# Kernel tuning notes

Hardware: AMD Instinct MI355X
Metric: run time of the kernel (lower is better)

Reference implementation:

```python
import jax, jax.numpy as jnp
import numpy as np
from jax import lax

H = 256      # hidden_size
B = 256      # batch
S = 672      # encoder history length (7 days of 15-min steps)
T = 96       # target_length (hardcoded TARGET_LENGTH)
IN = 1       # input_size


def _lstm_cell(x, h, c, Wih, Whh, b):
    # PyTorch gate order: i, f, g, o. b = b_ih + b_hh (combined).
    gates = x @ Wih.T + h @ Whh.T + b            # [B, 4H]
    i, f, g, o = jnp.split(gates, 4, axis=-1)
    c = jax.nn.sigmoid(f) * c + jax.nn.sigmoid(i) * jnp.tanh(g)
    h = jax.nn.sigmoid(o) * jnp.tanh(c)
    return h, c


def _run_lstm_layer(xs, Wih, Whh, b):
    # xs: [S, B, in] -> outputs [S, B, H], final (h, c)
    bsz = xs.shape[1]
    h0 = jnp.zeros((bsz, Whh.shape[1]), xs.dtype)
    c0 = jnp.zeros_like(h0)

    def step(carry, x):
        h, c = _lstm_cell(x, carry[0], carry[1], Wih, Whh, b)
        return (h, c), h

    (h, c), ys = lax.scan(step, (h0, c0), xs)
    return ys, h, c


def setup_inputs() -> dict:
    key = jax.random.key(0)
    ks = jax.random.split(key, 18)
    kscale = 1.0 / np.sqrt(H)

    def u(k, shape):
        return jax.random.uniform(k, shape, jnp.float32, -kscale, kscale)

    inp = {
        "features": jax.random.normal(ks[0], (B, S, IN), jnp.float32),
        # encoder LSTM (2 layers)
        "enc_Wih0": u(ks[1], (4 * H, IN)),
        "enc_Whh0": u(ks[2], (4 * H, H)),
        "enc_b0":   u(ks[3], (4 * H,)),
        "enc_Wih1": u(ks[4], (4 * H, H)),
        "enc_Whh1": u(ks[5], (4 * H, H)),
        "enc_b1":   u(ks[6], (4 * H,)),
        # decoder LSTM (2 layers, input size 1)
        "dec_Wih0": u(ks[7], (4 * H, 1)),
        "dec_Whh0": u(ks[8], (4 * H, H)),
        "dec_b0":   u(ks[9], (4 * H,)),
        "dec_Wih1": u(ks[10], (4 * H, H)),
        "dec_Whh1": u(ks[11], (4 * H, H)),
        "dec_b1":   u(ks[12], (4 * H,)),
        # output head: Linear(H,H) -> ReLU -> (Dropout=id at eval) -> Linear(H,1)
        "out_W1": u(ks[13], (H, H)),
        "out_b1": u(ks[14], (H,)),
        "out_W2": u(ks[15], (1, H)),
        "out_b2": u(ks[16], (1,)),
    }
    return inp


def reference(features, enc_Wih0, enc_Whh0, enc_b0, enc_Wih1, enc_Whh1, enc_b1,
              dec_Wih0, dec_Whh0, dec_b0, dec_Wih1, dec_Whh1, dec_b1,
              out_W1, out_b1, out_W2, out_b2):
    # --- encoder: 2-layer LSTM over the history ---
    xs = jnp.swapaxes(features, 0, 1)                       # [S, B, 1]
    ys0, eh0, ec0 = _run_lstm_layer(xs, enc_Wih0, enc_Whh0, enc_b0)
    _,   eh1, ec1 = _run_lstm_layer(ys0, enc_Wih1, enc_Whh1, enc_b1)

    x0 = jnp.zeros((features.shape[0], 1), features.dtype)  # [B, 1]

    def dec_step(carry, _):
        x, h0, c0, h1, c1 = carry
        h0, c0 = _lstm_cell(x, h0, c0, dec_Wih0, dec_Whh0, dec_b0)
        h1, c1 = _lstm_cell(h0, h1, c1, dec_Wih1, dec_Whh1, dec_b1)
        hid = jnp.maximum(h1 @ out_W1.T + out_b1, 0.0)      # ReLU (Dropout=id)
        pred = hid @ out_W2.T + out_b2                      # [B, 1]
        return (pred, h0, c0, h1, c1), pred[:, 0]

    _, preds = lax.scan(dec_step, (x0, eh0, ec0, eh1, ec1), None, length=T)
    return preds.T                                          # [B, T]
```

## Files before the change

kernel.cpp:

```cpp
#include <hip/hip_runtime.h>


#define S_LEN 672
#define T_LEN 96
#define HDIM  256
#define SPIN_MAX (1 << 14)

typedef short short8 __attribute__((ext_vector_type(8)));
typedef float f32x4  __attribute__((ext_vector_type(4)));
typedef unsigned short u16;

#define OFF_FLAG 0
#define OFF_FE   1024
#define OFF_FD   (OFF_FE + 16*8*32)
#define OFF_PART (OFF_FD + 16*16*32)
#define ZERO_END (OFF_PART + 2*16*256*4)
#define OFF_H0   ZERO_END
#define OFF_H1   (OFF_H0 + 16*2*4096*2)
#define OFF_F0   (OFF_H1 + 16*2*4096*2)
#define OFF_F1   (OFF_F0 + 16*4096*2)
#define OFF_C0   (OFF_F1 + 16*4096*2)
#define OFF_C1   (OFF_C0 + 256*256*4)

__device__ __forceinline__ unsigned short f2bf(float f) {
  unsigned u = __float_as_uint(f);
  u += 0x7FFFu + ((u >> 16) & 1u);
  return (unsigned short)(u >> 16);
}
__device__ __forceinline__ float bf2f(unsigned short s) {
  return __uint_as_float(((unsigned)s) << 16);
}
__device__ __forceinline__ float ld_scalar(const void* p, long idx, int mode) {
  if (mode) return bf2f(((const u16*)p)[idx]);
  return ((const float*)p)[idx];
}
__device__ __forceinline__ short8 ld_frag8(const void* p, long row, long ld, long k0, int mode) {
  if (mode) {
    return *(const short8*)((const u16*)p + row * ld + k0);
  } else {
    const float* f = (const float*)p + row * ld + k0;
    short8 r;
#pragma unroll
    for (int i = 0; i < 8; i++) r[i] = (short)f2bf(f[i]);
    return r;
  }
}
__device__ __forceinline__ void st_out(void* out, size_t idx, float v, int mode) {
  if (mode) ((u16*)out)[idx] = f2bf(v);
  else      ((float*)out)[idx] = v;
}
__device__ __forceinline__ float sigm(float x) { return 1.f / (1.f + __expf(-x)); }

__device__ __forceinline__ f32x4 mfma_bf16(short8 a, short8 b, f32x4 c) {
  return __builtin_amdgcn_mfma_f32_16x16x32_bf16(a, b, c, 0, 0, 0);
}

__device__ __forceinline__ void ld16B(const u16* b, short8* c0) {
  asm volatile("global_load_dwordx4 %0, %1, off sc0 sc1"
               : "=&v"(*c0) : "v"(b) : "memory");
}
__device__ __forceinline__ void ld32B(const u16* b, short8* c0, short8* c1) {
  asm volatile(
    "global_load_dwordx4 %0, %2, off sc0 sc1\n\t"
    "global_load_dwordx4 %1, %2, off offset:16 sc0 sc1"
    : "=&v"(*c0), "=&v"(*c1) : "v"(b) : "memory");
}
__device__ __forceinline__ void issue2(const u16* base, short8* t) {
  asm volatile(
    "global_load_dwordx4 %0, %2, off sc0 sc1\n\t"
    "global_load_dwordx4 %1, %2, off offset:64 sc0 sc1"
    : "=&v"(t[0]), "=&v"(t[1]) : "v"(base) : "memory");
}
__device__ __forceinline__ void st16(u16* p, unsigned short v) {
  asm volatile("global_store_short %0, %1, off sc0 sc1"
               :: "v"(p), "v"((unsigned)v) : "memory");
}
__device__ __forceinline__ void stf32(float* p, float v) {
  asm volatile("global_store_dword %0, %1, off sc0 sc1" :: "v"(p), "v"(v) : "memory");
}
__device__ __forceinline__ float ldf32(const float* p) {
  float v;
  asm volatile("global_load_dword %0, %1, off sc0 sc1\n\ts_waitcnt vmcnt(0)"
               : "=&v"(v) : "v"(p) : "memory");
  __builtin_amdgcn_sched_barrier(0);
  return v;
}
__device__ __forceinline__ void waitv0() {
  asm volatile("s_waitcnt vmcnt(0)" ::: "memory");
  __builtin_amdgcn_sched_barrier(0);
}

__device__ __forceinline__ void wg_publish(unsigned* fa, unsigned e) {
  asm volatile("s_waitcnt vmcnt(0)" ::: "memory");
  __syncthreads();
  if (threadIdx.x == 0)
    asm volatile("global_store_dword %0, %1, off sc0 sc1" :: "v"(fa), "v"(e) : "memory");
}
__device__ __forceinline__ void pollge8(const unsigned* flags, unsigned E) {
  const unsigned* addr = flags + (threadIdx.x & 7) * 8;
  int spin = 0;
  for (;;) {
    unsigned v;
    asm volatile("global_load_dword %0, %1, off sc0 sc1\n\ts_waitcnt vmcnt(0)"
                 : "=&v"(v) : "v"(addr) : "memory");
    if (__all(v >= E)) break;
    if (++spin > SPIN_MAX) break;
    __builtin_amdgcn_s_sleep(1);
  }
  __builtin_amdgcn_sched_barrier(0);
}
__device__ __forceinline__ void pollge16(const unsigned* flags, unsigned E) {
  const unsigned* addr = flags + (threadIdx.x & 15) * 8;
  int spin = 0;
  for (;;) {
    unsigned v;
    asm volatile("global_load_dword %0, %1, off sc0 sc1\n\ts_waitcnt vmcnt(0)"
                 : "=&v"(v) : "v"(addr) : "memory");
    if (__all(v >= E)) break;
    if (++spin > SPIN_MAX) break;
    __builtin_amdgcn_s_sleep(1);
  }
  __builtin_amdgcn_sched_barrier(0);
}

__global__ void detect_mode(const unsigned* __restrict__ feat, unsigned* __restrict__ flag) {
  const int t = threadIdx.x;
  int cnt = 0;
#pragma unroll
  for (int i = 0; i < 8; i++) {
    const unsigned wv = feat[t * 8 + i];
    const unsigned e = (wv >> 7) & 0xFFu;
    cnt += (e >= 100u && e <= 130u) ? 1 : 0;
  }
#pragma unroll
  for (int o = 32; o > 0; o >>= 1) cnt += __shfl_down(cnt, o, 64);
  if (t == 0) flag[0] = (cnt >= 256) ? 1u : 0u;
}

__global__ void __launch_bounds__(512, 1)
enc_kernel(const void* __restrict__ feat,
           const void* __restrict__ Wih0, const void* __restrict__ Whh0, const void* __restrict__ b0,
           const void* __restrict__ Wih1, const void* __restrict__ Whh1, const void* __restrict__ b1,
           char* __restrict__ ws) {
  const int mode = (int)*(const unsigned*)(ws + OFF_FLAG);
  const int tid  = threadIdx.x;
  const int lane = tid & 63;
  const int w    = tid >> 6;
  const int wl   = w & 3;
  const int bId  = blockIdx.x;
  const int g    = (bId & 7) * 2 + ((bId >> 3) & 1);
  const int m    = bId >> 4;
  const int sh   = m * 2 + (w >> 2);

  const int fcol = lane & 15;
  const int kq   = lane >> 4;
  const int chq  = sh * 16 + wl * 4 + kq;
  const int bgl  = g * 16 + fcol;
  const int sr   = tid >> 5;
  const int scc  = tid & 31;

  unsigned* fe_g = (unsigned*)(ws + OFF_FE) + g * 64;
  u16* h0s = (u16*)(ws + OFF_H0) + (size_t)g * 2 * 4096;
  u16* h1s = (u16*)(ws + OFF_H1) + (size_t)g * 2 * 4096;
  u16* f0s = (u16*)(ws + OFF_F0) + (size_t)g * 4096;
  u16* f1s = (u16*)(ws + OFF_F1) + (size_t)g * 4096;
  float* c0ws = (float*)(ws + OFF_C0);
  float* c1ws = (float*)(ws + OFF_C1);

  __shared__ short8 sh0[16][33];
  __shared__ short8 sh1[16][33];

  const int n    = 16 * wl + fcol;
  const int grow = (n & 3) * HDIM + sh * 16 + (n >> 2);
  short8 wh0[8], wi1[8], wh1[8];
#pragma unroll
  for (int kf = 0; kf < 8; kf++) {
    const int k0 = kf * 32 + kq * 8;
    wh0[kf] = ld_frag8(Whh0, grow, HDIM, k0, mode);
    wi1[kf] = ld_frag8(Wih1, grow, HDIM, k0, mode);
    wh1[kf] = ld_frag8(Whh1, grow, HDIM, k0, mode);
  }
  float wx[4], bb0[4], bb1[4];
#pragma unroll
  for (int gt = 0; gt < 4; gt++) {
    wx[gt]  = ld_scalar(Wih0, gt * HDIM + chq, mode);
    bb0[gt] = ld_scalar(b0,   gt * HDIM + chq, mode);
    bb1[gt] = ld_scalar(b1,   gt * HDIM + chq, mode);
  }
  float c0 = 0.f, c1 = 0.f, h0keep = 0.f, h1fin = 0.f;

  for (int t = 0; t <= S_LEN; t++) {
    const int pr = (t + 1) & 1, pw = t & 1;
    short8 a0[8], a1[8];
    if (t >= 1) {
      pollge8(fe_g, (unsigned)t);
      short8 va, vb;
      ld16B(h0s + pr * 4096 + tid * 8, &va);
      if (t >= 2) ld16B(h1s + pr * 4096 + tid * 8, &vb);
      waitv0();
      sh0[sr][scc] = va;
      if (t >= 2) sh1[sr][scc] = vb;
      __syncthreads();
#pragma unroll
      for (int kf = 0; kf < 8; kf++) a0[kf] = sh0[fcol][kf * 4 + kq];
      if (t >= 2) {
#pragma unroll
        for (int kf = 0; kf < 8; kf++) a1[kf] = sh1[fcol][kf * 4 + kq];
      }
    }

    f32x4 acc0 = {0.f, 0.f, 0.f, 0.f}, acc1 = {0.f, 0.f, 0.f, 0.f};
    if (t >= 1 && t < S_LEN) {
#pragma unroll
      for (int kf = 0; kf < 8; kf++) acc0 = mfma_bf16(wh0[kf], a0[kf], acc0);
    }
    if (t >= 1) {
#pragma unroll
      for (int kf = 0; kf < 8; kf++) acc1 = mfma_bf16(wi1[kf], a0[kf], acc1);
      if (t >= 2) {
#pragma unroll
        for (int kf = 0; kf < 8; kf++) acc1 = mfma_bf16(wh1[kf], a1[kf], acc1);
      }
    }
    if (t < S_LEN) {
      const float x = ld_scalar(feat, (long)bgl * S_LEN + t, mode);
      const float gi = acc0[0] + x * wx[0] + bb0[0];
      const float gf = acc0[1] + x * wx[1] + bb0[1];
      const float gg = acc0[2] + x * wx[2] + bb0[2];
      const float go = acc0[3] + x * wx[3] + bb0[3];
      c0 = sigm(gf) * c0 + sigm(gi) * tanhf(gg);
      const float h0v = sigm(go) * tanhf(c0);
      h0keep = h0v;
      st16(h0s + pw * 4096 + fcol * 256 + chq, f2bf(h0v));
    }
    if (t >= 1) {
      const float gi = acc1[0] + bb1[0];
      const float gf = acc1[1] + bb1[1];
      const float gg = acc1[2] + bb1[2];
      const float go = acc1[3] + bb1[3];
      c1 = sigm(gf) * c1 + sigm(gi) * tanhf(gg);
      const float h1v = sigm(go) * tanhf(c1);
      if (t < S_LEN) st16(h1s + pw * 4096 + fcol * 256 + chq, f2bf(h1v));
      else h1fin = h1v;
    }
    wg_publish(fe_g + m * 8, (unsigned)(t + 1));
  }
  f0s[fcol * 256 + chq] = f2bf(h0keep);
  f1s[fcol * 256 + chq] = f2bf(h1fin);
  c0ws[(size_t)bgl * HDIM + chq] = c0;
  c1ws[(size_t)bgl * HDIM + chq] = c1;
}

__global__ void __launch_bounds__(256, 1)
dec_kernel(const void* __restrict__ Wih0, const void* __restrict__ Whh0, const void* __restrict__ b0,
           const void* __restrict__ Wih1, const void* __restrict__ Whh1, const void* __restrict__ b1,
           const void* __restrict__ W1, const void* __restrict__ b1h, const void* __restrict__ W2,
           const void* __restrict__ b2, char* __restrict__ ws, void* __restrict__ out) {
  const int mode = (int)*(const unsigned*)(ws + OFF_FLAG);
  const int tid  = threadIdx.x;
  const int lane = tid & 63;
  const int w    = tid >> 6;
  const int bId  = blockIdx.x;
  const int g    = (bId & 7) * 2 + ((bId >> 3) & 1);
  const int m    = bId >> 4;

  const int fcol = lane & 15;
  const int kq   = lane >> 4;
  const int chq  = m * 16 + w * 4 + kq;
  const int bgl  = g * 16 + fcol;
  const int sr   = tid >> 4;
  const int sc2  = (tid & 15) * 2;

  unsigned* fd_g = (unsigned*)(ws + OFF_FD) + g * 128;
  u16* h0s = (u16*)(ws + OFF_H0) + (size_t)g * 2 * 4096;
  u16* h1s = (u16*)(ws + OFF_H1) + (size_t)g * 2 * 4096;
  u16* f0s = (u16*)(ws + OFF_F0) + (size_t)g * 4096;
  u16* f1s = (u16*)(ws + OFF_F1) + (size_t)g * 4096;
  float* partial = (float*)(ws + OFF_PART);
  float* c0ws = (float*)(ws + OFF_C0);
  float* c1ws = (float*)(ws + OFF_C1);

  __shared__ short8 sh0[16][33];
  __shared__ short8 sh1[16][33];
  __shared__ float part[4 * 256];
  __shared__ float redv[256];
  __shared__ float xacc[256];

  const int n    = 16 * w + fcol;
  const int grow = (n & 3) * HDIM + m * 16 + (n >> 2);
  short8 wh0[8], wi1[8], wh1[8], ww1[2];
#pragma unroll
  for (int kf = 0; kf < 8; kf++) {
    const int k0 = kf * 32 + kq * 8;
    wh0[kf] = ld_frag8(Whh0, grow, HDIM, k0, mode);
    wi1[kf] = ld_frag8(Wih1, grow, HDIM, k0, mode);
    wh1[kf] = ld_frag8(Whh1, grow, HDIM, k0, mode);
  }
#pragma unroll
  for (int kf2 = 0; kf2 < 2; kf2++) {
    const int k0 = w * 64 + kf2 * 32 + kq * 8;
    ww1[kf2] = ld_frag8(W1, m * 16 + fcol, HDIM, k0, mode);
  }
  float wx[4], bb0[4], bb1[4];
#pragma unroll
  for (int gt = 0; gt < 4; gt++) {
    wx[gt]  = ld_scalar(Wih0, gt * HDIM + chq, mode);
    bb0[gt] = ld_scalar(b0,   gt * HDIM + chq, mode);
    bb1[gt] = ld_scalar(b1,   gt * HDIM + chq, mode);
  }
  const int hb = tid & 15, hcl = tid >> 4;
  const float b1hv = ld_scalar(b1h, m * 16 + hcl, mode);
  const float w2v  = ld_scalar(W2,  m * 16 + hcl, mode);
  const float b2v  = ld_scalar(b2, 0, mode);

  float c0 = c0ws[(size_t)bgl * HDIM + chq];
  float c1 = c1ws[(size_t)bgl * HDIM + chq];

  for (int s = 0; s < T_LEN; s++) {
    const int ppr = (s - 1) & 1, pcur = s & 1;
    float x = 0.f;
    {
      if (s > 0) pollge16(fd_g, (unsigned)(3 * s));
      short8 va0, va1;
      float pv = 0.f;
      if (s > 0) {
        ld32B(h0s + ppr * 4096 + tid * 16, &va0, &va1);
        pv = ldf32(partial + (((size_t)ppr * 16 + g) * 16 + (tid >> 4)) * 16 + (tid & 15));
      } else {
        ld32B(f0s + tid * 16, &va0, &va1);
        waitv0();
      }
      sh0[sr][sc2] = va0; sh0[sr][sc2 + 1] = va1;
      if (s > 0) xacc[(tid & 15) * 16 + (tid >> 4)] = pv;
      __syncthreads();
      if (s > 0) {
#pragma unroll
        for (int j = 0; j < 16; j++) x += xacc[fcol * 16 + j];
        if (m == 0 && tid < 16)
          st_out(out, (size_t)(g * 16 + tid) * T_LEN + (s - 1), x, mode);
      }
      short8 a0[8];
#pragma unroll
      for (int kf = 0; kf < 8; kf++) a0[kf] = sh0[fcol][kf * 4 + kq];
      f32x4 acc = {0.f, 0.f, 0.f, 0.f};
#pragma unroll
      for (int kf = 0; kf < 8; kf++) acc = mfma_bf16(wh0[kf], a0[kf], acc);
      const float gi = acc[0] + x * wx[0] + bb0[0];
      const float gf = acc[1] + x * wx[1] + bb0[1];
      const float gg = acc[2] + x * wx[2] + bb0[2];
      const float go = acc[3] + x * wx[3] + bb0[3];
      c0 = sigm(gf) * c0 + sigm(gi) * tanhf(gg);
      const float h0v = sigm(go) * tanhf(c0);
      st16(h0s + pcur * 4096 + fcol * 256 + chq, f2bf(h0v));
      wg_publish(fd_g + m * 8, (unsigned)(3 * s + 1));
    }
    {
      pollge16(fd_g, (unsigned)(3 * s + 1));
      short8 va0, va1, vb0, vb1;
      ld32B(h0s + pcur * 4096 + tid * 16, &va0, &va1);
      ld32B(((s == 0) ? f1s : (h1s + ppr * 4096)) + tid * 16, &vb0, &vb1);
      waitv0();
      sh0[sr][sc2] = va0; sh0[sr][sc2 + 1] = va1;
      sh1[sr][sc2] = vb0; sh1[sr][sc2 + 1] = vb1;
      __syncthreads();
      short8 ay[8], a1[8];
#pragma unroll
      for (int kf = 0; kf < 8; kf++) {
        ay[kf] = sh0[fcol][kf * 4 + kq];
        a1[kf] = sh1[fcol][kf * 4 + kq];
      }
      f32x4 acc = {0.f, 0.f, 0.f, 0.f};
#pragma unroll
      for (int kf = 0; kf < 8; kf++) {
        acc = mfma_bf16(wi1[kf], ay[kf], acc);
        acc = mfma_bf16(wh1[kf], a1[kf], acc);
      }
      const float gi = acc[0] + bb1[0];
      const float gf = acc[1] + bb1[1];
      const float gg = acc[2] + bb1[2];
      const float go = acc[3] + bb1[3];
      c1 = sigm(gf) * c1 + sigm(gi) * tanhf(gg);
      const float h1v = sigm(go) * tanhf(c1);
      st16(h1s + pcur * 4096 + fcol * 256 + chq, f2bf(h1v));
      wg_publish(fd_g + m * 8, (unsigned)(3 * s + 2));
    }
    {
      pollge16(fd_g, (unsigned)(3 * s + 2));
      short8 ah[2];
      issue2(h1s + pcur * 4096 + fcol * 256 + w * 64 + kq * 8, ah);
      waitv0();
      f32x4 acc = {0.f, 0.f, 0.f, 0.f};
      acc = mfma_bf16(ww1[0], ah[0], acc);
      acc = mfma_bf16(ww1[1], ah[1], acc);
      *(f32x4*)&part[w * 256 + fcol * 16 + kq * 4] = acc;
      __syncthreads();
      float hid = part[0 * 256 + hb * 16 + hcl] + part[1 * 256 + hb * 16 + hcl]
                + part[2 * 256 + hb * 16 + hcl] + part[3 * 256 + hb * 16 + hcl] + b1hv;
      hid = fmaxf(hid, 0.f);
      redv[hcl * 16 + hb] = hid * w2v;
      __syncthreads();
      if (tid < 16) {
        float a = (m == 0) ? b2v : 0.f;
#pragma unroll
        for (int cc = 0; cc < 16; cc++) a += redv[cc * 16 + tid];
        stf32(partial + (((size_t)pcur * 16 + g) * 16 + m) * 16 + tid, a);
      }
      wg_publish(fd_g + m * 8, (unsigned)(3 * s + 3));
    }
  }
  if (m == 0) {
    pollge16(fd_g, (unsigned)(3 * T_LEN));
    const float pv = ldf32(partial + (((size_t)1 * 16 + g) * 16 + (tid >> 4)) * 16 + (tid & 15));
    xacc[(tid & 15) * 16 + (tid >> 4)] = pv;
    __syncthreads();
    if (tid < 16) {
      float x = 0.f;
#pragma unroll
      for (int j = 0; j < 16; j++) x += xacc[tid * 16 + j];
      st_out(out, (size_t)(g * 16 + tid) * T_LEN + (T_LEN - 1), x, mode);
    }
  }
}

extern "C" void kernel_launch(void* const* d_in, const int* in_sizes, int n_in,
                              void* d_out, int out_size, void* d_ws, size_t ws_size,
                              hipStream_t stream) {
  char* ws = (char*)d_ws;
  hipMemsetAsync(ws, 0, ZERO_END, stream);
  detect_mode<<<1, 64, 0, stream>>>((const unsigned*)d_in[0], (unsigned*)(ws + OFF_FLAG));
  enc_kernel<<<128, 512, 0, stream>>>(d_in[0], d_in[1], d_in[2], d_in[3],
                                      d_in[4], d_in[5], d_in[6], ws);
  dec_kernel<<<256, 256, 0, stream>>>(d_in[7], d_in[8], d_in[9], d_in[10], d_in[11], d_in[12],
                                      d_in[13], d_in[14], d_in[15], d_in[16], ws, d_out);
}
```

Measured before the change: 2.756 ms.

## Embed step tags in hidden-state words to replace flag-based encoder synchronization

The encoder stops publishing per-workgroup step flags and polling them. Each bf16 hidden value is now stored as a 32-bit word with the step index in the high half. Readers load the data directly, check the tags with a workgroup-wide vote, and reload until every tag is current. This removes the store-fence-barrier-flag round trip and the separate poll on each step, at the cost of doubling the h-buffer traffic and adding repack work. Decoder pointers are adjusted for the wider layout; the decoder body is not visible, so whether its h accesses still match is unclear.

```diff
diff --git a/kernel.cpp b/kernel.cpp
--- a/kernel.cpp
+++ b/kernel.cpp
@@ -5,19 +5,20 @@
 #define T_LEN 96
 #define HDIM  256
 #define SPIN_MAX (1 << 14)
+#define VOTE_MAX (1 << 13)
 
 typedef short short8 __attribute__((ext_vector_type(8)));
 typedef float f32x4  __attribute__((ext_vector_type(4)));
+typedef unsigned u32x4 __attribute__((ext_vector_type(4)));
 typedef unsigned short u16;
 
 #define OFF_FLAG 0
-#define OFF_FE   1024
-#define OFF_FD   (OFF_FE + 16*8*32)
+#define OFF_FD   1024
 #define OFF_PART (OFF_FD + 16*16*32)
-#define ZERO_END (OFF_PART + 2*16*256*4)
-#define OFF_H0   ZERO_END
-#define OFF_H1   (OFF_H0 + 16*2*4096*2)
-#define OFF_F0   (OFF_H1 + 16*2*4096*2)
+#define OFF_H0   (OFF_PART + 2*16*256*4)
+#define OFF_H1   (OFF_H0 + 16*2*4096*4)
+#define ZERO_END (OFF_H1 + 16*2*4096*4)
+#define OFF_F0   ZERO_END
 #define OFF_F1   (OFF_F0 + 16*4096*2)
 #define OFF_C0   (OFF_F1 + 16*4096*2)
 #define OFF_C1   (OFF_C0 + 256*256*4)
@@ -50,14 +51,17 @@
   else      ((float*)out)[idx] = v;
 }
 __device__ __forceinline__ float sigm(float x) { return 1.f / (1.f + __expf(-x)); }
+__device__ __forceinline__ unsigned umn(unsigned a, unsigned b) { return a < b ? a : b; }
 
 __device__ __forceinline__ f32x4 mfma_bf16(short8 a, short8 b, f32x4 c) {
   return __builtin_amdgcn_mfma_f32_16x16x32_bf16(a, b, c, 0, 0, 0);
 }
 
-__device__ __forceinline__ void ld16B(const u16* b, short8* c0) {
-  asm volatile("global_load_dwordx4 %0, %1, off sc0 sc1"
-               : "=&v"(*c0) : "v"(b) : "memory");
+__device__ __forceinline__ void ld32Bu(const unsigned* b, u32x4* c0, u32x4* c1) {
+  asm volatile(
+    "global_load_dwordx4 %0, %2, off sc0 sc1\n\t"
+    "global_load_dwordx4 %1, %2, off offset:16 sc0 sc1"
+    : "=&v"(*c0), "=&v"(*c1) : "v"(b) : "memory");
 }
 __device__ __forceinline__ void ld32B(const u16* b, short8* c0, short8* c1) {
   asm volatile(
@@ -74,6 +78,9 @@
 __device__ __forceinline__ void st16(u16* p, unsigned short v) {
   asm volatile("global_store_short %0, %1, off sc0 sc1"
                :: "v"(p), "v"((unsigned)v) : "memory");
+}
+__device__ __forceinline__ void st32(unsigned* p, unsigned v) {
+  asm volatile("global_store_dword %0, %1, off sc0 sc1" :: "v"(p), "v"(v) : "memory");
 }
 __device__ __forceinline__ void stf32(float* p, float v) {
   asm volatile("global_store_dword %0, %1, off sc0 sc1" :: "v"(p), "v"(v) : "memory");
@@ -90,24 +97,26 @@
   __builtin_amdgcn_sched_barrier(0);
 }
 
+__device__ __forceinline__ unsigned umin8(u32x4 a, u32x4 b) {
+  unsigned m = umn(umn(a.x, a.y), umn(a.z, a.w));
+  m = umn(m, umn(umn(b.x, b.y), umn(b.z, b.w)));
+  return m;
+}
+union PU { u32x4 u; short8 s; };
+__device__ __forceinline__ short8 pack8(u32x4 a, u32x4 b) {
+  u32x4 r;
+  r.x = __builtin_amdgcn_perm(a.y, a.x, 0x05040100u);
+  r.y = __builtin_amdgcn_perm(a.w, a.z, 0x05040100u);
+  r.z = __builtin_amdgcn_perm(b.y, b.x, 0x05040100u);
+  r.w = __builtin_amdgcn_perm(b.w, b.z, 0x05040100u);
+  PU p; p.u = r; return p.s;
+}
+
 __device__ __forceinline__ void wg_publish(unsigned* fa, unsigned e) {
   asm volatile("s_waitcnt vmcnt(0)" ::: "memory");
   __syncthreads();
   if (threadIdx.x == 0)
     asm volatile("global_store_dword %0, %1, off sc0 sc1" :: "v"(fa), "v"(e) : "memory");
-}
-__device__ __forceinline__ void pollge8(const unsigned* flags, unsigned E) {
-  const unsigned* addr = flags + (threadIdx.x & 7) * 8;
-  int spin = 0;
-  for (;;) {
-    unsigned v;
-    asm volatile("global_load_dword %0, %1, off sc0 sc1\n\ts_waitcnt vmcnt(0)"
-                 : "=&v"(v) : "v"(addr) : "memory");
-    if (__all(v >= E)) break;
-    if (++spin > SPIN_MAX) break;
-    __builtin_amdgcn_s_sleep(1);
-  }
-  __builtin_amdgcn_sched_barrier(0);
 }
 __device__ __forceinline__ void pollge16(const unsigned* flags, unsigned E) {
   const unsigned* addr = flags + (threadIdx.x & 15) * 8;
@@ -159,9 +168,8 @@
   const int sr   = tid >> 5;
   const int scc  = tid & 31;
 
-  unsigned* fe_g = (unsigned*)(ws + OFF_FE) + g * 64;
-  u16* h0s = (u16*)(ws + OFF_H0) + (size_t)g * 2 * 4096;
-  u16* h1s = (u16*)(ws + OFF_H1) + (size_t)g * 2 * 4096;
+  unsigned* h0s = (unsigned*)(ws + OFF_H0) + (size_t)g * 2 * 4096;
+  unsigned* h1s = (unsigned*)(ws + OFF_H1) + (size_t)g * 2 * 4096;
   u16* f0s = (u16*)(ws + OFF_F0) + (size_t)g * 4096;
   u16* f1s = (u16*)(ws + OFF_F1) + (size_t)g * 4096;
   float* c0ws = (float*)(ws + OFF_C0);
@@ -193,17 +201,31 @@
     const int pr = (t + 1) & 1, pw = t & 1;
     short8 a0[8], a1[8];
     if (t >= 1) {
-      pollge8(fe_g, (unsigned)t);
-      short8 va, vb;
-      ld16B(h0s + pr * 4096 + tid * 8, &va);
-      if (t >= 2) ld16B(h1s + pr * 4096 + tid * 8, &vb);
+      const unsigned* p0 = h0s + pr * 4096 + tid * 8;
+      const unsigned* p1 = h1s + pr * 4096 + tid * 8;
+      const bool need1 = (t >= 2);
+      const unsigned T0 = (unsigned)t << 16;
+      const unsigned T1 = (unsigned)(t - 1) << 16;
+      u32x4 c0a, c0b, c1a, c1b;
+      ld32Bu(p0, &c0a, &c0b);
+      if (need1) ld32Bu(p1, &c1a, &c1b);
+      __syncthreads();
       waitv0();
-      sh0[sr][scc] = va;
-      if (t >= 2) sh1[sr][scc] = vb;
-      __syncthreads();
+      int spin = 0;
+      for (;;) {
+        int ok = (umin8(c0a, c0b) >= T0);
+        if (need1) ok = ok && (umin8(c1a, c1b) >= T1);
+        sh0[sr][scc] = pack8(c0a, c0b);
+        if (need1) sh1[sr][scc] = pack8(c1a, c1b);
+        if (__syncthreads_and(ok)) break;
+        if (++spin > VOTE_MAX) break;
+        ld32Bu(p0, &c0a, &c0b);
+        if (need1) ld32Bu(p1, &c1a, &c1b);
+        waitv0();
+      }
 #pragma unroll
       for (int kf = 0; kf < 8; kf++) a0[kf] = sh0[fcol][kf * 4 + kq];
-      if (t >= 2) {
+      if (need1) {
 #pragma unroll
         for (int kf = 0; kf < 8; kf++) a1[kf] = sh1[fcol][kf * 4 + kq];
       }
@@ -231,7 +253,7 @@
       c0 = sigm(gf) * c0 + sigm(gi) * tanhf(gg);
       const float h0v = sigm(go) * tanhf(c0);
       h0keep = h0v;
-      st16(h0s + pw * 4096 + fcol * 256 + chq, f2bf(h0v));
+      st32(h0s + pw * 4096 + fcol * 256 + chq, ((unsigned)(t + 1) << 16) | f2bf(h0v));
     }
     if (t >= 1) {
       const float gi = acc1[0] + bb1[0];
@@ -240,10 +262,10 @@
       const float go = acc1[3] + bb1[3];
       c1 = sigm(gf) * c1 + sigm(gi) * tanhf(gg);
       const float h1v = sigm(go) * tanhf(c1);
-      if (t < S_LEN) st16(h1s + pw * 4096 + fcol * 256 + chq, f2bf(h1v));
+      if (t < S_LEN)
+        st32(h1s + pw * 4096 + fcol * 256 + chq, ((unsigned)t << 16) | f2bf(h1v));
       else h1fin = h1v;
     }
-    wg_publish(fe_g + m * 8, (unsigned)(t + 1));
   }
   f0s[fcol * 256 + chq] = f2bf(h0keep);
   f1s[fcol * 256 + chq] = f2bf(h1fin);
@@ -272,8 +294,8 @@
   const int sc2  = (tid & 15) * 2;
 
   unsigned* fd_g = (unsigned*)(ws + OFF_FD) + g * 128;
-  u16* h0s = (u16*)(ws + OFF_H0) + (size_t)g * 2 * 4096;
-  u16* h1s = (u16*)(ws + OFF_H1) + (size_t)g * 2 * 4096;
+  u16* h0s = (u16*)((unsigned*)(ws + OFF_H0) + (size_t)g * 2 * 4096);
+  u16* h1s = (u16*)((unsigned*)(ws + OFF_H1) + (size_t)g * 2 * 4096);
   u16* f0s = (u16*)(ws + OFF_F0) + (size_t)g * 4096;
   u16* f1s = (u16*)(ws + OFF_F1) + (size_t)g * 4096;
   float* partial = (float*)(ws + OFF_PART);
```

After: 6.051 ms. 2.2x slower.
